# Kernel tuning notes

Measured on AMD Instinct MI355X. Metric: run time of the kernel, lower is better.

Reference implementation:

```python
import jax, jax.numpy as jnp
import numpy as np

N, E = 16384, 262144
NS_N, NV_N = 128, 64      # node irreps: 128x0e + 64x1o
NS_E, NV_E = 64, 32       # edge irreps: 64x0e + 32x1o
C_OH, LAT = 16, 128
DS, DV = 128, 64          # irreps_out: 128x0e + 64x1o
GS = DS + DV              # gate input scalars (128 act scalars + 64 gates)
SC = 2 * NS_N + NS_E      # 320 concatenated scalar channels
VC = 2 * NV_N + NV_E      # 160 concatenated l=1 channels
M0_IN = SC + VC           # 480 m=0 features into SO2 linear
M0_OUT = GS + DV          # 256 m=0 outputs
AVG_NEI = 16.0
EPS = 1e-8


def setup_inputs() -> dict:
    key = jax.random.key(0)
    ks = jax.random.split(key, 20)
    f = lambda k, s: jax.random.normal(k, s, dtype=jnp.float32)
    return dict(
        node_feat=f(ks[0], (N, NS_N + 3 * NV_N)),
        edge_feat=f(ks[1], (E, NS_E + 3 * NV_E)),
        edge_vec=f(ks[2], (E, 3)),
        latents=f(ks[3], (E, LAT)),
        node_onehot=jax.nn.one_hot(jax.random.randint(ks[4], (N,), 0, C_OH), C_OH, dtype=jnp.float32),
        ln_n_g0=jnp.ones(NS_N), ln_n_b0=jnp.zeros(NS_N), ln_n_g1=jnp.ones(NV_N),
        ln_e_g0=jnp.ones(NS_E), ln_e_b0=jnp.zeros(NS_E), ln_e_g1=jnp.ones(NV_E),
        W_m0=f(ks[5], (M0_IN, M0_OUT)),
        w_r=f(ks[6], (VC, DV)), w_i=f(ks[7], (VC, DV)),
        W_env=f(ks[8], (LAT, DS + DV)),
        Wp0=f(ks[9], (DS, DS)), bp0=jnp.zeros(DS), Wpv=f(ks[10], (DV, DV)),
        Wtp0=f(ks[11], (DS, C_OH, GS)), Wtp1=f(ks[12], (DV, C_OH, DV)),
        Wo0=f(ks[13], (DS, DS)), bo0=jnp.zeros(DS), Wov=f(ks[14], (DV, DV)),
        res_param=jnp.zeros(()),
        edge_index=jax.random.randint(ks[15], (2, E), 0, N),
    )


def _sep_ln(s, v, g0, b0, g1):
    # separable equivariant layer norm: LN on scalars, per-sample RMS on l=1 block
    mu = s.mean(-1, keepdims=True)
    var = jnp.mean((s - mu) ** 2, -1, keepdims=True)
    s = (s - mu) * jax.lax.rsqrt(var + EPS) * g0 + b0
    vvar = jnp.mean(v * v, axis=(-2, -1), keepdims=True)  # component norm, degree-balanced (single l=1)
    v = v * jax.lax.rsqrt(vvar + EPS) * g1[None, :, None]
    return s, v


def _edge_frame(vec):
    # orthonormal frame (a, e1, e2) with a along the edge
    a = vec * jax.lax.rsqrt(jnp.sum(vec * vec, -1, keepdims=True) + EPS)
    helper = jnp.where(jnp.abs(a[:, 2:3]) < 0.99,
                       jnp.array([0.0, 0.0, 1.0], dtype=vec.dtype),
                       jnp.array([1.0, 0.0, 0.0], dtype=vec.dtype))
    e1 = jnp.cross(helper, a)
    e1 = e1 * jax.lax.rsqrt(jnp.sum(e1 * e1, -1, keepdims=True) + EPS)
    e2 = jnp.cross(a, e1)
    return a, e1, e2


def reference(node_feat, edge_feat, edge_vec, latents, node_onehot,
              ln_n_g0, ln_n_b0, ln_n_g1, ln_e_g0, ln_e_b0, ln_e_g1,
              W_m0, w_r, w_i, W_env, Wp0, bp0, Wpv,
              Wtp0, Wtp1, Wo0, bo0, Wov, res_param, edge_index):
    src, dst = edge_index[0], edge_index[1]
    ns, nv = node_feat[:, :NS_N], node_feat[:, NS_N:].reshape(-1, NV_N, 3)
    es, ev = edge_feat[:, :NS_E], edge_feat[:, NS_E:].reshape(-1, NV_E, 3)
    ns, nv = _sep_ln(ns, nv, ln_n_g0, ln_n_b0, ln_n_g1)
    es, ev = _sep_ln(es, ev, ln_e_g0, ln_e_b0, ln_e_g1)
    # per-edge concat: node[src] + edge + node[dst]
    s_cat = jnp.concatenate([ns[src], es, ns[dst]], -1)          # [E, SC]
    v_cat = jnp.concatenate([nv[src], ev, nv[dst]], 1)           # [E, VC, 3]
    # SO2 linear: rotate into edge frame, mix per |m|, rotate back
    a, e1, e2 = _edge_frame(edge_vec)
    c0 = jnp.einsum('eci,ei->ec', v_cat, a)
    c1 = jnp.einsum('eci,ei->ec', v_cat, e1)
    c2 = jnp.einsum('eci,ei->ec', v_cat, e2)
    m0 = jnp.concatenate([s_cat, c0], -1) @ W_m0 * (1.0 / np.sqrt(M0_IN))  # [E, M0_OUT]
    s_out, c0o = m0[:, :GS], m0[:, GS:]
    inv = 1.0 / np.sqrt(VC)
    c1o = (c1 @ w_r - c2 @ w_i) * inv
    c2o = (c1 @ w_i + c2 @ w_r) * inv
    v_out = (c0o[..., None] * a[:, None, :] + c1o[..., None] * e1[:, None, :]
             + c2o[..., None] * e2[:, None, :])                  # [E, DV, 3]
    # gate activation
    s_act = jax.nn.silu(s_out[:, :DS])
    gates = jax.nn.sigmoid(s_out[:, DS:])
    v_g = v_out * gates[..., None]
    # lin_post (per-l linear, scalar bias)
    s2 = s_act @ Wp0 * (1.0 / np.sqrt(DS)) + bp0
    v2 = jnp.einsum('eui,uv->evi', v_g, Wpv) * (1.0 / np.sqrt(DV))
    # env weighting from latents (E3ElementLinear, per-irrep-channel scalars)
    w = latents @ W_env * (1.0 / np.sqrt(LAT))
    s2 = s2 * w[:, :DS]
    v2 = v2 * w[:, DS:, None]
    nrm = 1.0 / np.sqrt(AVG_NEI)
    sa = jax.ops.segment_sum(s2, dst, num_segments=N) * nrm
    va = jax.ops.segment_sum(v2, dst, num_segments=N) * nrm
    # one-hot FullyConnectedTensorProduct (in2 all 0e) + gate + linear
    t0 = jnp.einsum('nu,nc,ucv->nv', sa, node_onehot, Wtp0) * (1.0 / np.sqrt(DS * C_OH))
    t1 = jnp.einsum('nui,nc,ucv->nvi', va, node_onehot, Wtp1) * (1.0 / np.sqrt(DV * C_OH))
    s3 = jax.nn.silu(t0[:, :DS])
    v3 = t1 * jax.nn.sigmoid(t0[:, DS:])[..., None]
    s4 = s3 @ Wo0 * (1.0 / np.sqrt(DS)) + bo0
    v4 = jnp.einsum('nui,uv->nvi', v3, Wov) * (1.0 / np.sqrt(DV))
    new = jnp.concatenate([s4, v4.reshape(-1, 3 * DV)], -1)
    r = jax.nn.sigmoid(res_param)
    return r * node_feat + (1.0 - r) * new
```

## Files before the change

kernel.cpp:

```cpp
#include <hip/hip_runtime.h>
#include <math.h>

#define N_NODES 16384
#define N_EDGES 262144
#define EPSF 1e-8f

#define OFF_XE    0
#define OFF_C12   14848
#define OFF_FR    35840
#define OFF_EDST  36608
#define OFF_ESRC  36736
#define POOL_BYTES 36864
#define OFF_SACT  0
#define OFF_GATE  8704
#define OFF_C0O   13312
#define OFF_C1O   17920
#define OFF_C2O   22528
#define OFF_VG    8704

typedef __bf16 bf16x8 __attribute__((ext_vector_type(8)));
typedef float  f32x4  __attribute__((ext_vector_type(4)));

__device__ __forceinline__ f32x4 MFMA16(bf16x8 a, bf16x8 b, f32x4 c){
  return __builtin_amdgcn_mfma_f32_16x16x32_bf16(a, b, c, 0, 0, 0);
}

__device__ __forceinline__ unsigned short f2bf(float x){
  __bf16 h = (__bf16)x;
  union { __bf16 b; unsigned short u; } c; c.b = h;
  return c.u;
}
__device__ __forceinline__ float bf2f(unsigned short h){
  union { unsigned u; float f; } c; c.u = ((unsigned)h)<<16;
  return c.f;
}
__device__ __forceinline__ float wsum64(float v){
  #pragma unroll
  for (int m=1; m<64; m<<=1) v += __shfl_xor(v, m);
  return v;
}
__device__ __forceinline__ float wsum32(float v){
  #pragma unroll
  for (int m=1; m<32; m<<=1) v += __shfl_xor(v, m);
  return v;
}
__device__ __forceinline__ float sigm(float x){ return 1.0f/(1.0f+__expf(-x)); }
__device__ __forceinline__ float silu(float x){ return x/(1.0f+__expf(-x)); }

__global__ __launch_bounds__(256) void k_pack_all(
  const float* __restrict__ Wm0, const float* __restrict__ wr,
  const float* __restrict__ wi,  const float* __restrict__ Wenv,
  const float* __restrict__ Wp0, const float* __restrict__ Wpv,
  unsigned short* __restrict__ wpk)
{
  int i = blockIdx.x*256 + threadIdx.x;
  if (i < 122880){
    int k = i >> 8, n = i & 255;
    int idx = (((k>>5)*256 + n)*4 + ((k>>3)&3))*8 + (k&7);
    wpk[idx] = f2bf(Wm0[i]);
  } else if (i < 163840){
    int j = i - 122880;
    int k = j >> 7, n = j & 127;
    float v;
    if (k < 160) v = (n < 64) ? wr[k*64 + n]        : wi[k*64 + (n-64)];
    else         v = (n < 64) ? -wi[(k-160)*64 + n] : wr[(k-160)*64 + (n-64)];
    int idx = (((k>>5)*128 + n)*4 + ((k>>3)&3))*8 + (k&7);
    wpk[122880 + idx] = f2bf(v);
  } else if (i < 188416){
    int j = i - 163840;
    int k = j / 192, n = j - k*192;
    int idx = (((k>>5)*192 + n)*4 + ((k>>3)&3))*8 + (k&7);
    wpk[163840 + idx] = f2bf(Wenv[j]);
  } else if (i < 204800){
    int j = i - 188416;
    int k = j >> 7, n = j & 127;
    int idx = (((k>>5)*128 + n)*4 + ((k>>3)&3))*8 + (k&7);
    wpk[188416 + idx] = f2bf(Wp0[j]);
  } else if (i < 208896){
    int j = i - 204800;
    int k = j >> 6, n = j & 63;
    int idx = (((k>>5)*64 + n)*4 + ((k>>3)&3))*8 + (k&7);
    wpk[204800 + idx] = f2bf(Wpv[j]);
  }
}

__global__ __launch_bounds__(256) void k_hist(const int* __restrict__ eidx, int* __restrict__ cnt){
  int e = blockIdx.x*256 + threadIdx.x;
  if (e < N_EDGES) atomicAdd(&cnt[eidx[N_EDGES+e]], 1);
}
__global__ __launch_bounds__(256) void k_scan(const int* __restrict__ cnt,
                                              int* __restrict__ rowp, int* __restrict__ cursor){
  __shared__ int part[256];
  __shared__ int pref[257];
  const int t = threadIdx.x;
  const int base = t*64;
  int s = 0;
  for (int i=0;i<64;i++) s += cnt[base+i];
  part[t] = s; __syncthreads();
  if (t==0){ int a=0; for (int i=0;i<256;i++){ pref[i]=a; a+=part[i]; } pref[256]=a; }
  __syncthreads();
  int a = pref[t];
  for (int i=0;i<64;i++){ rowp[base+i]=a; cursor[base+i]=a; a += cnt[base+i]; }
  if (t==0) rowp[N_NODES] = pref[256];
}
__global__ __launch_bounds__(256) void k_fill(const int* __restrict__ eidx,
                                              int* __restrict__ cursor, int* __restrict__ perm){
  int e = blockIdx.x*256 + threadIdx.x;
  if (e < N_EDGES){
    int pos = atomicAdd(&cursor[eidx[N_EDGES+e]], 1);
    perm[pos] = e;
  }
}

__global__ __launch_bounds__(256) void k_node_ln(
    const float* __restrict__ nf, const float* __restrict__ g0,
    const float* __restrict__ b0, const float* __restrict__ g1,
    unsigned short* __restrict__ ns_ln, _Float16* __restrict__ nv_ln)
{
  const int tid  = threadIdx.x;
  const int lane = tid & 63;
  const int n    = blockIdx.x*4 + (tid>>6);
  const float* row = nf + (size_t)n*320;

  float s0 = row[lane], s1 = row[64+lane];
  float mu = wsum64(s0+s1) * (1.0f/128.0f);
  float d0 = s0-mu, d1 = s1-mu;
  float var = wsum64(d0*d0+d1*d1) * (1.0f/128.0f);
  float rs = rsqrtf(var + EPSF);
  ns_ln[(size_t)n*128 + lane]    = f2bf(d0*rs*g0[lane]    + b0[lane]);
  ns_ln[(size_t)n*128 + 64+lane] = f2bf(d1*rs*g0[64+lane] + b0[64+lane]);

  float px = row[128+lane*3+0], py = row[128+lane*3+1], pz = row[128+lane*3+2];
  float vvar = wsum64(px*px+py*py+pz*pz) * (1.0f/192.0f);
  float vsc = rsqrtf(vvar + EPSF) * g1[lane];
  nv_ln[(size_t)n*192 + lane*3+0] = (_Float16)(px*vsc);
  nv_ln[(size_t)n*192 + lane*3+1] = (_Float16)(py*vsc);
  nv_ln[(size_t)n*192 + lane*3+2] = (_Float16)(pz*vsc);
}

__global__ __launch_bounds__(256) void k_wenv(
  const float* __restrict__ lats, const unsigned short* __restrict__ pWenv,
  const int* __restrict__ perm, unsigned short* __restrict__ wbuf)
{
  __shared__ unsigned short A[64*136];
  const int tid = threadIdx.x;
  {
    const int row = tid>>2, part = tid&3;
    const int slot = blockIdx.x*64 + row;
    const int e = perm[slot];
    const float* lr = lats + (size_t)e*128 + part*32;
    #pragma unroll
    for (int q=0;q<8;q++){
      float4 v = *(const float4*)(lr + q*4);
      int cb = part*32 + q*4;
      A[row*136 + cb+0] = f2bf(v.x);
      A[row*136 + cb+1] = f2bf(v.y);
      A[row*136 + cb+2] = f2bf(v.z);
      A[row*136 + cb+3] = f2bf(v.w);
    }
  }
  __syncthreads();
  const int wid = tid>>6, l = tid&63, r15 = l&15, g = l>>4;
  const f32x4 zero4 = {0.f,0.f,0.f,0.f};
  f32x4 acc[4][3];
  #pragma unroll
  for (int m=0;m<4;m++)
    #pragma unroll
    for (int n=0;n<3;n++) acc[m][n]=zero4;

  const unsigned short* bbase = pWenv + ((size_t)(wid*48 + r15)*4 + g)*8;
  #pragma unroll
  for (int kc=0;kc<4;kc++){
    bf16x8 b[3];
    #pragma unroll
    for (int n=0;n<3;n++) b[n] = *(const bf16x8*)(bbase + (size_t)kc*6144 + n*512);
    #pragma unroll
    for (int m=0;m<4;m++){
      bf16x8 a = *(const bf16x8*)&A[(m*16+r15)*136 + kc*32 + g*8];
      #pragma unroll
      for (int n=0;n<3;n++) acc[m][n] = MFMA16(a, b[n], acc[m][n]);
    }
  }
  #pragma unroll
  for (int m=0;m<4;m++)
    #pragma unroll
    for (int n=0;n<3;n++)
      #pragma unroll
      for (int r=0;r<4;r++){
        int sr = m*16 + g*4 + r;
        int j  = wid*48 + n*16 + r15;
        wbuf[(size_t)(blockIdx.x*64 + sr)*192 + j] = f2bf(acc[m][n][r]*0.08838834764831845f);
      }
}

__global__ __launch_bounds__(256,4) void k_edge(
  const float* __restrict__ ef, const float* __restrict__ evec,
  const float* __restrict__ g0e, const float* __restrict__ b0e, const float* __restrict__ g1e,
  const unsigned short* __restrict__ pWm0, const unsigned short* __restrict__ pWc,
  const unsigned short* __restrict__ pWp0, const unsigned short* __restrict__ pWpv,
  const float* __restrict__ bp0,
  const int* __restrict__ eidx, const int* __restrict__ perm,
  const unsigned short* __restrict__ ns_ln, const _Float16* __restrict__ nv_ln,
  const unsigned short* __restrict__ wbuf,
  float* __restrict__ sa, float* __restrict__ va)
{
  extern __shared__ unsigned char pool[];
  const int tid = threadIdx.x;
  unsigned short* XE   = (unsigned short*)(pool + OFF_XE);
  unsigned short* C12s = (unsigned short*)(pool + OFF_C12);
  _Float16* FRh = (_Float16*)(pool + OFF_FR);
  int* EDST = (int*)(pool + OFF_EDST);
  int* ESRC = (int*)(pool + OFF_ESRC);

  const int nwg = gridDim.x;
  const int bswz = (blockIdx.x & 7)*(nwg>>3) + (blockIdx.x >> 3);

  const int wid = tid>>6, l = tid&63;
  const int r15 = l&15, g = l>>4;
  const int sbase = bswz*32;

  {
    const int ln = tid & 31;
    #pragma unroll
    for (int eo=0; eo<4; ++eo){
      const int el = eo*8 + (tid>>5);
      const int slot = sbase + el;
      const size_t e = (size_t)perm[slot];
      const int src = eidx[e];
      const int dst = eidx[N_EDGES + e];

      float vx=evec[e*3+0], vy=evec[e*3+1], vz=evec[e*3+2];
      float rn = rsqrtf(vx*vx+vy*vy+vz*vz+EPSF);
      float ax=vx*rn, ay=vy*rn, az=vz*rn;
      float hx, hz;
      if (fabsf(az) < 0.99f){ hx=0.f; hz=1.f; } else { hx=1.f; hz=0.f; }
      float e1x = -hz*ay;
      float e1y = hz*ax - hx*az;
      float e1z = hx*ay;
      float rn1 = rsqrtf(e1x*e1x+e1y*e1y+e1z*e1z+EPSF);
      e1x*=rn1; e1y*=rn1; e1z*=rn1;
      float e2x = ay*e1z - az*e1y;
      float e2y = az*e1x - ax*e1z;
      float e2z = ax*e1y - ay*e1x;
      if (ln==0){
        FRh[el*12+0]=(_Float16)ax;  FRh[el*12+1]=(_Float16)ay;  FRh[el*12+2]=(_Float16)az;
        FRh[el*12+3]=(_Float16)e1x; FRh[el*12+4]=(_Float16)e1y; FRh[el*12+5]=(_Float16)e1z;
        FRh[el*12+6]=(_Float16)e2x; FRh[el*12+7]=(_Float16)e2y; FRh[el*12+8]=(_Float16)e2z;
        EDST[el]=dst;
        ESRC[el]=src;
      }

      const float* erow = ef + e*160;
      float s0=erow[ln], s1=erow[32+ln];
      float mu = wsum32(s0+s1)*(1.f/64.f);
      float d0=s0-mu, d1=s1-mu;
      float var = wsum32(d0*d0+d1*d1)*(1.f/64.f);
      float rs = rsqrtf(var+EPSF);
      XE[el*232 + ln]    = f2bf(d0*rs*g0e[ln]    + b0e[ln]);
      XE[el*232 + 32+ln] = f2bf(d1*rs*g0e[32+ln] + b0e[32+ln]);

      float wx=erow[64+ln*3+0], wy=erow[64+ln*3+1], wz=erow[64+ln*3+2];
      float vvar = wsum32(wx*wx+wy*wy+wz*wz)*(1.f/96.f);
      float vsc = rsqrtf(vvar+EPSF)*g1e[ln];
      wx*=vsc; wy*=vsc; wz*=vsc;
      XE  [el*232 + 64+64+ln]    = f2bf(wx*ax +wy*ay +wz*az);
      C12s[el*328 + 64+ln]       = f2bf(wx*e1x+wy*e1y+wz*e1z);
      C12s[el*328 + 160+64+ln]   = f2bf(wx*e2x+wy*e2y+wz*e2z);

      const _Float16* nvs = nv_ln + (size_t)src*192;
      const _Float16* nvd = nv_ln + (size_t)dst*192;
      #pragma unroll
      for (int q=0;q<2;q++){
        int u = ln+32*q;
        float px=(float)nvs[u*3+0], py=(float)nvs[u*3+1], pz=(float)nvs[u*3+2];
        XE  [el*232 + 64+u]      = f2bf(px*ax +py*ay +pz*az);
        C12s[el*328 + u]         = f2bf(px*e1x+py*e1y+pz*e1z);
        C12s[el*328 + 160+u]     = f2bf(px*e2x+py*e2y+pz*e2z);
        px=(float)nvd[u*3+0]; py=(float)nvd[u*3+1]; pz=(float)nvd[u*3+2];
        XE  [el*232 + 64+96+u]   = f2bf(px*ax +py*ay +pz*az);
        C12s[el*328 + 96+u]      = f2bf(px*e1x+py*e1y+pz*e1z);
        C12s[el*328 + 160+96+u]  = f2bf(px*e2x+py*e2y+pz*e2z);
      }
    }
  }
  __syncthreads();

  const f32x4 zero4 = {0.f,0.f,0.f,0.f};

  f32x4 acc1[2][4];
  #pragma unroll
  for (int m=0;m<2;m++)
    #pragma unroll
    for (int n=0;n<4;n++) acc1[m][n]=zero4;

  {
    const unsigned short* bbase = pWm0 + ((size_t)(wid*64 + r15)*4 + g)*8;
    bf16x8 gA[2][8];
    {
      const int rs0 = ESRC[r15], rs1 = ESRC[16+r15];
      const int rd0 = EDST[r15], rd1 = EDST[16+r15];
      #pragma unroll
      for (int q=0;q<4;q++){
        gA[0][q]   = *(const bf16x8*)&ns_ln[(size_t)rs0*128 + q*32 + g*8];
        gA[1][q]   = *(const bf16x8*)&ns_ln[(size_t)rs1*128 + q*32 + g*8];
        gA[0][4+q] = *(const bf16x8*)&ns_ln[(size_t)rd0*128 + q*32 + g*8];
        gA[1][4+q] = *(const bf16x8*)&ns_ln[(size_t)rd1*128 + q*32 + g*8];
      }
    }
    #pragma unroll
    for (int t=0;t<7;t++){
      const int kc  = (t<2) ? (4+t) : (10 + t-2);
      const int col = (t<2) ? (t*32) : (64 + (t-2)*32);
      bf16x8 a0 = *(const bf16x8*)&XE[(    r15)*232 + col + g*8];
      bf16x8 a1 = *(const bf16x8*)&XE[(16+ r15)*232 + col + g*8];
      const unsigned short* bp = bbase + (size_t)kc*8192;
      #pragma unroll
      for (int n=0;n<4;n++){
        bf16x8 b = *(const bf16x8*)(bp + n*512);
        acc1[0][n] = MFMA16(a0,b,acc1[0][n]);
        acc1[1][n] = MFMA16(a1,b,acc1[1][n]);
      }
    }
    #pragma unroll
    for (int t=0;t<8;t++){
      const int kc = (t<4) ? t : (6 + t-4);
      const unsigned short* bp = bbase + (size_t)kc*8192;
      #pragma unroll
      for (int n=0;n<4;n++){
        bf16x8 b = *(const bf16x8*)(bp + n*512);
        acc1[0][n] = MFMA16(gA[0][t],b,acc1[0][n]);
        acc1[1][n] = MFMA16(gA[1][t],b,acc1[1][n]);
      }
    }
  }

  f32x4 acc2[2][2];
  #pragma unroll
  for (int m=0;m<2;m++){ acc2[m][0]=zero4; acc2[m][1]=zero4; }
  {
    const unsigned short* bbase = pWc + ((size_t)(wid*32 + r15)*4 + g)*8;
    #pragma unroll
    for (int kc=0;kc<10;kc++){
      bf16x8 a0 = *(const bf16x8*)&C12s[(    r15)*328 + kc*32 + g*8];
      bf16x8 a1 = *(const bf16x8*)&C12s[(16+ r15)*328 + kc*32 + g*8];
      const unsigned short* bp = bbase + (size_t)kc*4096;
      #pragma unroll
      for (int n=0;n<2;n++){
        bf16x8 b = *(const bf16x8*)(bp + n*512);
        acc2[0][n] = MFMA16(a0,b,acc2[0][n]);
        acc2[1][n] = MFMA16(a1,b,acc2[1][n]);
      }
    }
  }

  float wsc[2][2][4], wvc[2][4], bp0v[2];
  #pragma unroll
  for (int n=0;n<2;n++) bp0v[n] = bp0[wid*32 + n*16 + r15];
  #pragma unroll
  for (int m=0;m<2;m++)
    #pragma unroll
    for (int r=0;r<4;r++){
      int e = m*16 + g*4 + r;
      #pragma unroll
      for (int n=0;n<2;n++)
        wsc[m][n][r] = bf2f(wbuf[(size_t)(sbase+e)*192 + wid*32 + n*16 + r15]);
      wvc[m][r] = bf2f(wbuf[(size_t)(sbase+e)*192 + 128 + wid*16 + r15]);
    }

  __syncthreads();

  {
    unsigned short* SAs = (unsigned short*)(pool + OFF_SACT);
    unsigned short* GAb = (unsigned short*)(pool + OFF_GATE);
    unsigned short* C0b = (unsigned short*)(pool + OFF_C0O);
    #pragma unroll
    for (int m=0;m<2;m++)
      #pragma unroll
      for (int n=0;n<4;n++)
        #pragma unroll
        for (int r=0;r<4;r++){
          int e = m*16 + g*4 + r;
          int j = wid*64 + n*16 + r15;
          float v = acc1[m][n][r]*0.04564354645876384f;
          if (j < 128)      SAs[e*136 + j] = f2bf(silu(v));
          else if (j < 192) GAb[e*72 + (j-128)] = f2bf(sigm(v));
          else              C0b[e*72 + (j-192)] = f2bf(v);
        }
    unsigned short* C1b = (unsigned short*)(pool + OFF_C1O);
    unsigned short* C2b = (unsigned short*)(pool + OFF_C2O);
    #pragma unroll
    for (int m=0;m<2;m++)
      #pragma unroll
      for (int n=0;n<2;n++)
        #pragma unroll
        for (int r=0;r<4;r++){
          int e = m*16 + g*4 + r;
          int j = wid*32 + n*16 + r15;
          float v = acc2[m][n][r]*0.07905694150420949f;
          if (j < 64) C1b[e*72 + j] = f2bf(v);
          else        C2b[e*72 + (j-64)] = f2bf(v);
        }
  }
  __syncthreads();

  {
    const int e = tid>>3, u0 = (tid&7)*8;
    const unsigned short* GAb = (const unsigned short*)(pool + OFF_GATE);
    const unsigned short* C0b = (const unsigned short*)(pool + OFF_C0O);
    const unsigned short* C1b = (const unsigned short*)(pool + OFF_C1O);
    const unsigned short* C2b = (const unsigned short*)(pool + OFF_C2O);
    float ax=(float)FRh[e*12+0],  ay=(float)FRh[e*12+1],  az=(float)FRh[e*12+2];
    float b1x=(float)FRh[e*12+3], b1y=(float)FRh[e*12+4], b1z=(float)FRh[e*12+5];
    float b2x=(float)FRh[e*12+6], b2y=(float)FRh[e*12+7], b2z=(float)FRh[e*12+8];
    float vgx[8], vgy[8], vgz[8];
    #pragma unroll
    for (int i=0;i<8;i++){
      int u = u0+i;
      float gt = bf2f(GAb[e*72+u]);
      float c0 = bf2f(C0b[e*72+u]), c1 = bf2f(C1b[e*72+u]), c2 = bf2f(C2b[e*72+u]);
      vgx[i] = (c0*ax + c1*b1x + c2*b2x)*gt;
      vgy[i] = (c0*ay + c1*b1y + c2*b2y)*gt;
      vgz[i] = (c0*az + c1*b1z + c2*b2z)*gt;
    }
    __syncthreads();
    unsigned short* VGs = (unsigned short*)(pool + OFF_VG);
    #pragma unroll
    for (int i=0;i<8;i++){
      VGs[0*2304 + e*72 + u0+i] = f2bf(vgx[i]);
      VGs[1*2304 + e*72 + u0+i] = f2bf(vgy[i]);
      VGs[2*2304 + e*72 + u0+i] = f2bf(vgz[i]);
    }
  }
  __syncthreads();

  {
    const unsigned short* SAs = (const unsigned short*)(pool + OFF_SACT);
    const unsigned short* VGs = (const unsigned short*)(pool + OFF_VG);

    f32x4 acc4[2][2], acc5[3][2];
    #pragma unroll
    for (int m=0;m<2;m++){ acc4[m][0]=zero4; acc4[m][1]=zero4; }
    #pragma unroll
    for (int c=0;c<3;c++){ acc5[c][0]=zero4; acc5[c][1]=zero4; }

    {
      const unsigned short* bbase = pWp0 + ((size_t)(wid*32 + r15)*4 + g)*8;
      #pragma unroll
      for (int kc=0;kc<4;kc++){
        bf16x8 a0 = *(const bf16x8*)&SAs[(    r15)*136 + kc*32 + g*8];
        bf16x8 a1 = *(const bf16x8*)&SAs[(16+ r15)*136 + kc*32 + g*8];
        #pragma unroll
        for (int n=0;n<2;n++){
          bf16x8 b = *(const bf16x8*)(bbase + (size_t)kc*4096 + n*512);
          acc4[0][n] = MFMA16(a0,b,acc4[0][n]);
          acc4[1][n] = MFMA16(a1,b,acc4[1][n]);
        }
      }
    }
    {
      bf16x8 b5[2];
      #pragma unroll
      for (int kc=0;kc<2;kc++)
        b5[kc] = *(const bf16x8*)(pWpv + ((size_t)(kc*64 + wid*16 + r15)*4 + g)*8);
      #pragma unroll
      for (int c=0;c<3;c++)
        #pragma unroll
        for (int kc=0;kc<2;kc++){
          bf16x8 a0 = *(const bf16x8*)&VGs[c*2304 + (    r15)*72 + kc*32 + g*8];
          bf16x8 a1 = *(const bf16x8*)&VGs[c*2304 + (16+ r15)*72 + kc*32 + g*8];
          acc5[c][0] = MFMA16(a0,b5[kc],acc5[c][0]);
          acc5[c][1] = MFMA16(a1,b5[kc],acc5[c][1]);
        }
    }

    __syncthreads();
    _Float16* R = (_Float16*)pool;
    #pragma unroll
    for (int m=0;m<2;m++)
      #pragma unroll
      for (int n=0;n<2;n++)
        #pragma unroll
        for (int r=0;r<4;r++){
          int e = m*16 + g*4 + r;
          int j = wid*32 + n*16 + r15;
          R[e*320 + j] = (_Float16)((acc4[m][n][r]*0.08838834764831845f + bp0v[n]) * wsc[m][n][r]);
        }
    #pragma unroll
    for (int c=0;c<3;c++)
      #pragma unroll
      for (int m=0;m<2;m++)
        #pragma unroll
        for (int r=0;r<4;r++){
          int e = m*16 + g*4 + r;
          int vch = wid*16 + r15;
          R[e*320 + 128 + vch*3 + c] = (_Float16)(acc5[c][m][r]*0.125f * wvc[m][r]);
        }
    __syncthreads();

    for (int j = tid; j < 320; j += 256){
      float accv = (float)R[j];
      int cur = EDST[0];
      for (int e=1;e<32;e++){
        int d = EDST[e];
        float v = (float)R[e*320 + j];
        if (d != cur){
          float* tgt = (j<128) ? &sa[(size_t)cur*128 + j] : &va[(size_t)cur*192 + (j-128)];
          atomicAdd(tgt, accv);
          accv = v; cur = d;
        } else accv += v;
      }
      float* tgt = (j<128) ? &sa[(size_t)cur*128 + j] : &va[(size_t)cur*192 + (j-128)];
      atomicAdd(tgt, accv);
    }
  }
}

__global__ __launch_bounds__(256) void k_node_out(
  const float* __restrict__ nf, const float* __restrict__ oh,
  const float* __restrict__ Wtp0, const float* __restrict__ Wtp1,
  const float* __restrict__ Wo0, const float* __restrict__ bo0,
  const float* __restrict__ Wov, const float* __restrict__ resp,
  const float* __restrict__ sa, const float* __restrict__ va,
  float* __restrict__ out)
{
  __shared__ float SAB[4][128];
  __shared__ float VX[4][64], VY[4][64], VZ[4][64];
  __shared__ float S3 [4][128];
  __shared__ float V3 [4][256];
  const int tid=threadIdx.x, lane=tid&63, g=tid>>6;
  const int n = blockIdx.x*4 + g;

  float cf=0.f;
  #pragma unroll
  for (int j=0;j<16;j++) cf += j*oh[(size_t)n*16+j];
  const int c = (int)(cf+0.5f);

  SAB[g][lane]    = sa[(size_t)n*128+lane]   *0.25f;
  SAB[g][64+lane] = sa[(size_t)n*128+64+lane]*0.25f;
  VX[g][lane] = va[(size_t)n*192+lane*3+0]*0.25f;
  VY[g][lane] = va[(size_t)n*192+lane*3+1]*0.25f;
  VZ[g][lane] = va[(size_t)n*192+lane*3+2]*0.25f;
  __syncthreads();

  float t00=0.f, t01=0.f, t02=0.f;
  const float* w0c = Wtp0 + (size_t)c*192;
  for (int u=0;u<128;u++){
    float s = SAB[g][u];
    t00 += s * w0c[(size_t)u*3072 + lane];
    t01 += s * w0c[(size_t)u*3072 + lane+64];
    t02 += s * w0c[(size_t)u*3072 + lane+128];
  }
  const float sct0 = 0.02209708691f;
  t00*=sct0; t01*=sct0; t02*=sct0;

  float t1x=0.f,t1y=0.f,t1z=0.f;
  const float* w1c = Wtp1 + (size_t)c*64;
  for (int u=0;u<64;u++){
    float wv = w1c[(size_t)u*1024 + lane];
    t1x += VX[g][u]*wv;
    t1y += VY[g][u]*wv;
    t1z += VZ[g][u]*wv;
  }
  t1x*=0.03125f; t1y*=0.03125f; t1z*=0.03125f;

  S3[g][lane]    = silu(t00);
  S3[g][64+lane] = silu(t01);
  float g2 = sigm(t02);
  float4 v3v = {t1x*g2, t1y*g2, t1z*g2, 0.f};
  *(float4*)&V3[g][lane*4] = v3v;
  __syncthreads();

  float s40=0.f, s41=0.f;
  for (int k=0;k<128;k++){
    float s3k = S3[g][k];
    s40 += s3k*Wo0[k*128+lane];
    s41 += s3k*Wo0[k*128+64+lane];
  }
  s40 = s40*0.08838834765f + bo0[lane];
  s41 = s41*0.08838834765f + bo0[64+lane];

  float v4x=0.f,v4y=0.f,v4z=0.f;
  for (int u=0;u<64;u++){
    float4 v3u = *(const float4*)&V3[g][u*4];
    float wv = Wov[u*64+lane];
    v4x += v3u.x*wv; v4y += v3u.y*wv; v4z += v3u.z*wv;
  }
  v4x*=0.125f; v4y*=0.125f; v4z*=0.125f;

  const float r = sigm(resp[0]);
  const float* row = nf + (size_t)n*320;
  float* orow = out + (size_t)n*320;
  orow[lane]      = r*row[lane]      + (1.f-r)*s40;
  orow[64+lane]   = r*row[64+lane]   + (1.f-r)*s41;
  orow[128+lane*3+0] = r*row[128+lane*3+0] + (1.f-r)*v4x;
  orow[128+lane*3+1] = r*row[128+lane*3+1] + (1.f-r)*v4y;
  orow[128+lane*3+2] = r*row[128+lane*3+2] + (1.f-r)*v4z;
}

extern "C" void kernel_launch(void* const* d_in, const int* in_sizes, int n_in,
                              void* d_out, int out_size, void* d_ws, size_t ws_size,
                              hipStream_t stream)
{
  const float* nf   = (const float*)d_in[0];
  const float* ef   = (const float*)d_in[1];
  const float* evec = (const float*)d_in[2];
  const float* lats = (const float*)d_in[3];
  const float* oh   = (const float*)d_in[4];
  const float* g0n  = (const float*)d_in[5];
  const float* b0n  = (const float*)d_in[6];
  const float* g1n  = (const float*)d_in[7];
  const float* g0e  = (const float*)d_in[8];
  const float* b0e  = (const float*)d_in[9];
  const float* g1e  = (const float*)d_in[10];
  const float* Wm0  = (const float*)d_in[11];
  const float* wr   = (const float*)d_in[12];
  const float* wi   = (const float*)d_in[13];
  const float* Wenv = (const float*)d_in[14];
  const float* Wp0  = (const float*)d_in[15];
  const float* bp0  = (const float*)d_in[16];
  const float* Wpv  = (const float*)d_in[17];
  const float* Wtp0 = (const float*)d_in[18];
  const float* Wtp1 = (const float*)d_in[19];
  const float* Wo0  = (const float*)d_in[20];
  const float* bo0  = (const float*)d_in[21];
  const float* Wov  = (const float*)d_in[22];
  const float* resp = (const float*)d_in[23];
  const int*   eidx = (const int*)d_in[24];

  char* base = (char*)d_ws;
  unsigned short* ns_ln = (unsigned short*)(base);
  _Float16* nv_ln = (_Float16*)(base + 4194304);
  float* sa    = (float*)(base + 10485760);
  float* va    = (float*)(base + 18874368);
  unsigned short* wpk = (unsigned short*)(base + 31457280);
  unsigned short* pWm0  = wpk;
  unsigned short* pWc   = wpk + 122880;
  unsigned short* pWenv = wpk + 163840;
  unsigned short* pWp0  = wpk + 188416;
  unsigned short* pWpv  = wpk + 204800;
  int* ibuf   = (int*)(base + 31875072);
  int* cnt    = ibuf;
  int* rowp   = ibuf + 16384;
  int* cursor = ibuf + 32769;
  int* perm   = ibuf + 49153;
  unsigned short* wbuf = (unsigned short*)(base + 33120264);

  hipMemsetAsync(sa, 0, (size_t)N_NODES*320*sizeof(float), stream);
  hipMemsetAsync(cnt, 0, N_NODES*sizeof(int), stream);

  k_pack_all<<<(208896+255)/256, 256, 0, stream>>>(Wm0, wr, wi, Wenv, Wp0, Wpv, wpk);
  k_node_ln<<<N_NODES/4, 256, 0, stream>>>(nf, g0n, b0n, g1n, ns_ln, nv_ln);

  k_hist<<<(N_EDGES+255)/256, 256, 0, stream>>>(eidx, cnt);
  k_scan<<<1, 256, 0, stream>>>(cnt, rowp, cursor);
  k_fill<<<(N_EDGES+255)/256, 256, 0, stream>>>(eidx, cursor, perm);

  k_wenv<<<N_EDGES/64, 256, 0, stream>>>(lats, pWenv, perm, wbuf);

  k_edge<<<N_EDGES/32, 256, POOL_BYTES, stream>>>(ef, evec, g0e, b0e, g1e,
                                                  pWm0, pWc, pWp0, pWpv, bp0,
                                                  eidx, perm, ns_ln, nv_ln, wbuf,
                                                  sa, va);
  k_node_out<<<N_NODES/4, 256, 0, stream>>>(nf, oh, Wtp0, Wtp1, Wo0, bo0, Wov,
                                            resp, sa, va, (float*)d_out);
}
```

Measured before the change: 587.6 us.

## Fuse latent env-weight GEMM into edge kernel and vectorize edge gathers

Removes the separate k_wenv kernel. Each edge block now computes its latents @ W_env product with MFMA, converting latents to bf16 in registers, and keeps the result in a new LDS region instead of writing and re-reading a global bf16 buffer. The edge-feature LN and node l=1 gathers are rewritten to use wider float2/float4/uint2 loads and packed bf16 stores, and VG stores are packed two per word. In exchange the LDS pool grows and launch bounds drop from 4 to 3 blocks per CU, which may lower occupancy.

```diff
diff --git a/kernel.cpp b/kernel.cpp
--- a/kernel.cpp
+++ b/kernel.cpp
@@ -10,7 +10,8 @@
 #define OFF_FR    35840
 #define OFF_EDST  36608
 #define OFF_ESRC  36736
-#define POOL_BYTES 36864
+#define OFF_WENV  36864
+#define POOL_BYTES 49664
 #define OFF_SACT  0
 #define OFF_GATE  8704
 #define OFF_C0O   13312
@@ -25,23 +26,23 @@
   return __builtin_amdgcn_mfma_f32_16x16x32_bf16(a, b, c, 0, 0, 0);
 }
 
-__device__ __forceinline__ unsigned short f2bf(float x){
+__device__ __forceinline__ unsigned f2bf(float x){
   __bf16 h = (__bf16)x;
   union { __bf16 b; unsigned short u; } c; c.b = h;
-  return c.u;
+  return (unsigned)c.u;
 }
 __device__ __forceinline__ float bf2f(unsigned short h){
   union { unsigned u; float f; } c; c.u = ((unsigned)h)<<16;
   return c.f;
 }
+__device__ __forceinline__ float wsum32(float v){
+  #pragma unroll
+  for (int m=1; m<32; m<<=1) v += __shfl_xor(v, m);
+  return v;
+}
 __device__ __forceinline__ float wsum64(float v){
   #pragma unroll
   for (int m=1; m<64; m<<=1) v += __shfl_xor(v, m);
-  return v;
-}
-__device__ __forceinline__ float wsum32(float v){
-  #pragma unroll
-  for (int m=1; m<32; m<<=1) v += __shfl_xor(v, m);
   return v;
 }
 __device__ __forceinline__ float sigm(float x){ return 1.0f/(1.0f+__expf(-x)); }
@@ -138,70 +139,16 @@
   nv_ln[(size_t)n*192 + lane*3+2] = (_Float16)(pz*vsc);
 }
 
-__global__ __launch_bounds__(256) void k_wenv(
-  const float* __restrict__ lats, const unsigned short* __restrict__ pWenv,
-  const int* __restrict__ perm, unsigned short* __restrict__ wbuf)
-{
-  __shared__ unsigned short A[64*136];
-  const int tid = threadIdx.x;
-  {
-    const int row = tid>>2, part = tid&3;
-    const int slot = blockIdx.x*64 + row;
-    const int e = perm[slot];
-    const float* lr = lats + (size_t)e*128 + part*32;
-    #pragma unroll
-    for (int q=0;q<8;q++){
-      float4 v = *(const float4*)(lr + q*4);
-      int cb = part*32 + q*4;
-      A[row*136 + cb+0] = f2bf(v.x);
-      A[row*136 + cb+1] = f2bf(v.y);
-      A[row*136 + cb+2] = f2bf(v.z);
-      A[row*136 + cb+3] = f2bf(v.w);
-    }
-  }
-  __syncthreads();
-  const int wid = tid>>6, l = tid&63, r15 = l&15, g = l>>4;
-  const f32x4 zero4 = {0.f,0.f,0.f,0.f};
-  f32x4 acc[4][3];
-  #pragma unroll
-  for (int m=0;m<4;m++)
-    #pragma unroll
-    for (int n=0;n<3;n++) acc[m][n]=zero4;
-
-  const unsigned short* bbase = pWenv + ((size_t)(wid*48 + r15)*4 + g)*8;
-  #pragma unroll
-  for (int kc=0;kc<4;kc++){
-    bf16x8 b[3];
-    #pragma unroll
-    for (int n=0;n<3;n++) b[n] = *(const bf16x8*)(bbase + (size_t)kc*6144 + n*512);
-    #pragma unroll
-    for (int m=0;m<4;m++){
-      bf16x8 a = *(const bf16x8*)&A[(m*16+r15)*136 + kc*32 + g*8];
-      #pragma unroll
-      for (int n=0;n<3;n++) acc[m][n] = MFMA16(a, b[n], acc[m][n]);
-    }
-  }
-  #pragma unroll
-  for (int m=0;m<4;m++)
-    #pragma unroll
-    for (int n=0;n<3;n++)
-      #pragma unroll
-      for (int r=0;r<4;r++){
-        int sr = m*16 + g*4 + r;
-        int j  = wid*48 + n*16 + r15;
-        wbuf[(size_t)(blockIdx.x*64 + sr)*192 + j] = f2bf(acc[m][n][r]*0.08838834764831845f);
-      }
-}
-
-__global__ __launch_bounds__(256,4) void k_edge(
+__global__ __launch_bounds__(256,3) void k_edge(
   const float* __restrict__ ef, const float* __restrict__ evec,
+  const float* __restrict__ lats,
   const float* __restrict__ g0e, const float* __restrict__ b0e, const float* __restrict__ g1e,
   const unsigned short* __restrict__ pWm0, const unsigned short* __restrict__ pWc,
-  const unsigned short* __restrict__ pWp0, const unsigned short* __restrict__ pWpv,
+  const unsigned short* __restrict__ pWenv, const unsigned short* __restrict__ pWp0,
+  const unsigned short* __restrict__ pWpv,
   const float* __restrict__ bp0,
   const int* __restrict__ eidx, const int* __restrict__ perm,
   const unsigned short* __restrict__ ns_ln, const _Float16* __restrict__ nv_ln,
-  const unsigned short* __restrict__ wbuf,
   float* __restrict__ sa, float* __restrict__ va)
 {
   extern __shared__ unsigned char pool[];
@@ -211,6 +158,7 @@
   _Float16* FRh = (_Float16*)(pool + OFF_FR);
   int* EDST = (int*)(pool + OFF_EDST);
   int* ESRC = (int*)(pool + OFF_ESRC);
+  unsigned short* WEs = (unsigned short*)(pool + OFF_WENV);
 
   const int nwg = gridDim.x;
   const int bswz = (blockIdx.x & 7)*(nwg>>3) + (blockIdx.x >> 3);
@@ -251,35 +199,80 @@
       }
 
       const float* erow = ef + e*160;
-      float s0=erow[ln], s1=erow[32+ln];
-      float mu = wsum32(s0+s1)*(1.f/64.f);
-      float d0=s0-mu, d1=s1-mu;
-      float var = wsum32(d0*d0+d1*d1)*(1.f/64.f);
-      float rs = rsqrtf(var+EPSF);
-      XE[el*232 + ln]    = f2bf(d0*rs*g0e[ln]    + b0e[ln]);
-      XE[el*232 + 32+ln] = f2bf(d1*rs*g0e[32+ln] + b0e[32+ln]);
-
-      float wx=erow[64+ln*3+0], wy=erow[64+ln*3+1], wz=erow[64+ln*3+2];
-      float vvar = wsum32(wx*wx+wy*wy+wz*wz)*(1.f/96.f);
-      float vsc = rsqrtf(vvar+EPSF)*g1e[ln];
-      wx*=vsc; wy*=vsc; wz*=vsc;
-      XE  [el*232 + 64+64+ln]    = f2bf(wx*ax +wy*ay +wz*az);
-      C12s[el*328 + 64+ln]       = f2bf(wx*e1x+wy*e1y+wz*e1z);
-      C12s[el*328 + 160+64+ln]   = f2bf(wx*e2x+wy*e2y+wz*e2z);
-
-      const _Float16* nvs = nv_ln + (size_t)src*192;
-      const _Float16* nvd = nv_ln + (size_t)dst*192;
-      #pragma unroll
-      for (int q=0;q<2;q++){
-        int u = ln+32*q;
-        float px=(float)nvs[u*3+0], py=(float)nvs[u*3+1], pz=(float)nvs[u*3+2];
-        XE  [el*232 + 64+u]      = f2bf(px*ax +py*ay +pz*az);
-        C12s[el*328 + u]         = f2bf(px*e1x+py*e1y+pz*e1z);
-        C12s[el*328 + 160+u]     = f2bf(px*e2x+py*e2y+pz*e2z);
-        px=(float)nvd[u*3+0]; py=(float)nvd[u*3+1]; pz=(float)nvd[u*3+2];
-        XE  [el*232 + 64+96+u]   = f2bf(px*ax +py*ay +pz*az);
-        C12s[el*328 + 96+u]      = f2bf(px*e1x+py*e1y+pz*e1z);
-        C12s[el*328 + 160+96+u]  = f2bf(px*e2x+py*e2y+pz*e2z);
+
+      {
+        float2 sp = *(const float2*)&erow[2*ln];
+        float mu = wsum32(sp.x+sp.y)*(1.f/64.f);
+        float d0=sp.x-mu, d1=sp.y-mu;
+        float var = wsum32(d0*d0+d1*d1)*(1.f/64.f);
+        float rs = rsqrtf(var+EPSF);
+        float2 gv = *(const float2*)&g0e[2*ln];
+        float2 bv = *(const float2*)&b0e[2*ln];
+        unsigned lo = f2bf(d0*rs*gv.x + bv.x);
+        unsigned hi = f2bf(d1*rs*gv.y + bv.y);
+        *(unsigned*)&XE[el*232 + 2*ln] = lo | (hi<<16);
+      }
+
+      {
+        float evb[12];
+        float evq = 0.f;
+        if (ln < 8){
+          float4 p0 = *(const float4*)&erow[64 + ln*12];
+          float4 p1 = *(const float4*)&erow[64 + ln*12 + 4];
+          float4 p2 = *(const float4*)&erow[64 + ln*12 + 8];
+          evb[0]=p0.x; evb[1]=p0.y; evb[2]=p0.z; evb[3]=p0.w;
+          evb[4]=p1.x; evb[5]=p1.y; evb[6]=p1.z; evb[7]=p1.w;
+          evb[8]=p2.x; evb[9]=p2.y; evb[10]=p2.z; evb[11]=p2.w;
+          #pragma unroll
+          for (int i=0;i<12;i++) evq += evb[i]*evb[i];
+        }
+        float vvar = wsum32(evq)*(1.f/96.f);
+        float vsce = rsqrtf(vvar+EPSF);
+        if (ln < 8){
+          unsigned xw[2]={0,0}, c1w[2]={0,0}, c2w[2]={0,0};
+          #pragma unroll
+          for (int i=0;i<4;i++){
+            float s = vsce * g1e[ln*4+i];
+            float wx=evb[3*i]*s, wy=evb[3*i+1]*s, wz=evb[3*i+2]*s;
+            unsigned c0 = f2bf(wx*ax +wy*ay +wz*az);
+            unsigned c1 = f2bf(wx*e1x+wy*e1y+wz*e1z);
+            unsigned c2 = f2bf(wx*e2x+wy*e2y+wz*e2z);
+            int w = i>>1, sh = (i&1)*16;
+            xw[w] |= c0<<sh; c1w[w] |= c1<<sh; c2w[w] |= c2<<sh;
+          }
+          uint2 xv={xw[0],xw[1]}, c1v={c1w[0],c1w[1]}, c2v={c2w[0],c2w[1]};
+          *(uint2*)&XE  [el*232 + 128 + ln*4]      = xv;
+          *(uint2*)&C12s[el*328 + 64 + ln*4]       = c1v;
+          *(uint2*)&C12s[el*328 + 160 + 64 + ln*4] = c2v;
+        }
+      }
+
+      {
+        const int isrc = (ln < 16);
+        const int u0 = (ln & 15)*4;
+        const int node = isrc ? src : dst;
+        const _Float16* nvp = nv_ln + (size_t)node*192 + u0*3;
+        union { uint2 u2; _Float16 h[4]; } nb0, nb1, nb2;
+        nb0.u2 = *(const uint2*)(nvp);
+        nb1.u2 = *(const uint2*)(nvp+4);
+        nb2.u2 = *(const uint2*)(nvp+8);
+        _Float16 hh[12];
+        *(uint2*)&hh[0] = nb0.u2; *(uint2*)&hh[4] = nb1.u2; *(uint2*)&hh[8] = nb2.u2;
+        unsigned xw[2]={0,0}, c1w[2]={0,0}, c2w[2]={0,0};
+        #pragma unroll
+        for (int i=0;i<4;i++){
+          float px=(float)hh[3*i], py=(float)hh[3*i+1], pz=(float)hh[3*i+2];
+          unsigned c0 = f2bf(px*ax +py*ay +pz*az);
+          unsigned c1 = f2bf(px*e1x+py*e1y+pz*e1z);
+          unsigned c2 = f2bf(px*e2x+py*e2y+pz*e2z);
+          int w = i>>1, sh = (i&1)*16;
+          xw[w] |= c0<<sh; c1w[w] |= c1<<sh; c2w[w] |= c2<<sh;
+        }
+        const int cb = isrc ? u0 : (96 + u0);
+        uint2 xv={xw[0],xw[1]}, c1v={c1w[0],c1w[1]}, c2v={c2w[0],c2w[1]};
+        *(uint2*)&XE  [el*232 + 64 + cb]  = xv;
+        *(uint2*)&C12s[el*328 + cb]       = c1v;
+        *(uint2*)&C12s[el*328 + 160 + cb] = c2v;
       }
     }
   }
@@ -292,7 +285,6 @@
   for (int m=0;m<2;m++)
     #pragma unroll
     for (int n=0;n<4;n++) acc1[m][n]=zero4;
-
   {
     const unsigned short* bbase = pWm0 + ((size_t)(wid*64 + r15)*4 + g)*8;
     bf16x8 gA[2][8];
@@ -353,6 +345,49 @@
     }
   }
 
+  {
+    f32x4 acc3[2][3];
+    #pragma unroll
+    for (int m=0;m<2;m++)
+      #pragma unroll
+      for (int n=0;n<3;n++) acc3[m][n]=zero4;
+    const int eA0 = perm[sbase + r15];
+    const int eA1 = perm[sbase + 16 + r15];
+    const float* la0 = lats + (size_t)eA0*128;
+    const float* la1 = lats + (size_t)eA1*128;
+    const unsigned short* bbase = pWenv + ((size_t)(wid*48 + r15)*4 + g)*8;
+    #pragma unroll
+    for (int kc=0;kc<4;kc++){
+      float4 f00 = *(const float4*)&la0[kc*32 + g*8];
+      float4 f01 = *(const float4*)&la0[kc*32 + g*8 + 4];
+      float4 f10 = *(const float4*)&la1[kc*32 + g*8];
+      float4 f11 = *(const float4*)&la1[kc*32 + g*8 + 4];
+      union { bf16x8 v; unsigned short s[8]; } a0, a1;
+      a0.s[0]=f2bf(f00.x); a0.s[1]=f2bf(f00.y); a0.s[2]=f2bf(f00.z); a0.s[3]=f2bf(f00.w);
+      a0.s[4]=f2bf(f01.x); a0.s[5]=f2bf(f01.y); a0.s[6]=f2bf(f01.z); a0.s[7]=f2bf(f01.w);
+      a1.s[0]=f2bf(f10.x); a1.s[1]=f2bf(f10.y); a1.s[2]=f2bf(f10.z); a1.s[3]=f2bf(f10.w);
+      a1.s[4]=f2bf(f11.x); a1.s[5]=f2bf(f11.y); a1.s[6]=f2bf(f11.z); a1.s[7]=f2bf(f11.w);
+      #pragma unroll
+      for (int n=0;n<3;n++){
+        bf16x8 b = *(const bf16x8*)(bbase + (size_t)kc*6144 + n*512);
+        acc3[0][n] = MFMA16(a0.v, b, acc3[0][n]);
+        acc3[1][n] = MFMA16(a1.v, b, acc3[1][n]);
+      }
+    }
+    #pragma unroll
+    for (int m=0;m<2;m++)
+      #pragma unroll
+      for (int n=0;n<3;n++)
+        #pragma unroll
+        for (int r=0;r<4;r++){
+          int e = m*16 + g*4 + r;
+          int j = wid*48 + n*16 + r15;
+          WEs[e*200 + j] = f2bf(acc3[m][n][r]*0.08838834764831845f);
+        }
+  }
+
+  __syncthreads();
+
   float wsc[2][2][4], wvc[2][4], bp0v[2];
   #pragma unroll
   for (int n=0;n<2;n++) bp0v[n] = bp0[wid*32 + n*16 + r15];
@@ -363,11 +398,9 @@
       int e = m*16 + g*4 + r;
       #pragma unroll
       for (int n=0;n<2;n++)
-        wsc[m][n][r] = bf2f(wbuf[(size_t)(sbase+e)*192 + wid*32 + n*16 + r15]);
-      wvc[m][r] = bf2f(wbuf[(size_t)(sbase+e)*192 + 128 + wid*16 + r15]);
-    }
-
-  __syncthreads();
+        wsc[m][n][r] = bf2f(WEs[e*200 + wid*32 + n*16 + r15]);
+      wvc[m][r] = bf2f(WEs[e*200 + 128 + wid*16 + r15]);
+    }
 
   {
     unsigned short* SAs = (unsigned short*)(pool + OFF_SACT);
@@ -425,10 +458,13 @@
     __syncthreads();
     unsigned short* VGs = (unsigned short*)(pool + OFF_VG);
     #pragma unroll
-    for (int i=0;i<8;i++){
-      VGs[0*2304 + e*72 + u0+i] = f2bf(vgx[i]);
-      VGs[1*2304 + e*72 + u0+i] = f2bf(vgy[i]);
-      VGs[2*2304 + e*72 + u0+i] = f2bf(vgz[i]);
+    for (int i=0;i<4;i++){
+      unsigned wx = f2bf(vgx[2*i]) | (f2bf(vgx[2*i+1])<<16);
+      unsigned wy = f2bf(vgy[2*i]) | (f2bf(vgy[2*i+1])<<16);
+      unsigned wz = f2bf(vgz[2*i]) | (f2bf(vgz[2*i+1])<<16);
+      *(unsigned*)&VGs[0*2304 + e*72 + u0 + 2*i] = wx;
+      *(unsigned*)&VGs[1*2304 + e*72 + u0 + 2*i] = wy;
+      *(unsigned*)&VGs[2*2304 + e*72 + u0 + 2*i] = wz;
     }
   }
   __syncthreads();
@@ -643,7 +679,6 @@
   int* rowp   = ibuf + 16384;
   int* cursor = ibuf + 32769;
   int* perm   = ibuf + 49153;
-  unsigned short* wbuf = (unsigned short*)(base + 33120264);
 
   hipMemsetAsync(sa, 0, (size_t)N_NODES*320*sizeof(float), stream);
   hipMemsetAsync(cnt, 0, N_NODES*sizeof(int), stream);
@@ -655,11 +690,9 @@
   k_scan<<<1, 256, 0, stream>>>(cnt, rowp, cursor);
   k_fill<<<(N_EDGES+255)/256, 256, 0, stream>>>(eidx, cursor, perm);
 
-  k_wenv<<<N_EDGES/64, 256, 0, stream>>>(lats, pWenv, perm, wbuf);
-
-  k_edge<<<N_EDGES/32, 256, POOL_BYTES, stream>>>(ef, evec, g0e, b0e, g1e,
-                                                  pWm0, pWc, pWp0, pWpv, bp0,
-                                                  eidx, perm, ns_ln, nv_ln, wbuf,
+  k_edge<<<N_EDGES/32, 256, POOL_BYTES, stream>>>(ef, evec, lats, g0e, b0e, g1e,
+                                                  pWm0, pWc, pWenv, pWp0, pWpv, bp0,
+                                                  eidx, perm, ns_ln, nv_ln,
                                                   sa, va);
   k_node_out<<<N_NODES/4, 256, 0, stream>>>(nf, oh, Wtp0, Wtp1, Wo0, bo0, Wov,
                                             resp, sa, va, (float*)d_out);
```

Measured after the change: 736.6 us. 25.4% more time.
